# Optimization experiments

Hardware: AMD Instinct MI355X
Metric: run time of the kernel (lower is better)

Reference implementation:

```python
import jax, jax.numpy as jnp
import numpy as np

# --- fake-quant helpers (Brevitas INT quantization, straight-through in bwd) ---

def quant_weight_2bit(w):
    # symmetric signed 2-bit, narrow range: integer levels {-1, 0, 1}
    qmax = 1.0
    s = jnp.max(jnp.abs(jax.lax.stop_gradient(w))) / qmax
    r = jnp.clip(jnp.round(w / s), -qmax, qmax) * s
    return w + jax.lax.stop_gradient(r - w)  # STE


def quant_relu_2bit(x, max_val=6.0):
    # unsigned 2-bit activation quant: levels {0, 1, 2, 3} scaled to [0, max_val]
    n = 3.0  # 2**2 - 1
    s = max_val / n
    y = jnp.clip(x, 0.0, max_val)  # relu + clamp at max_val
    r = jnp.round(y / s) * s
    return y + jax.lax.stop_gradient(r - y)  # STE


def conv3x3_same(x, w):
    # NCHW input, OIHW weight, stride 1, padding 1
    return jax.lax.conv_general_dilated(
        x, w, window_strides=(1, 1), padding=((1, 1), (1, 1)),
        dimension_numbers=("NCHW", "OIHW", "NCHW"))


def maxpool2x2(x):
    return jax.lax.reduce_window(
        x, -jnp.inf, jax.lax.max,
        window_dimensions=(1, 1, 2, 2), window_strides=(1, 1, 2, 2),
        padding="VALID")


def setup_inputs() -> dict:
    key = jax.random.key(0)
    k0, k1, k2, k3 = jax.random.split(key, 4)
    B = 32768
    x = jax.random.normal(k0, (B, 1, 28, 28), dtype=jnp.float32)
    w1 = jax.random.normal(k1, (4, 1, 3, 3), dtype=jnp.float32) * 0.3
    w2 = jax.random.normal(k2, (4, 4, 3, 3), dtype=jnp.float32) * 0.2
    wf = jax.random.normal(k3, (10, 4 * 7 * 7), dtype=jnp.float32) * 0.1
    return {"x": x, "w1": w1, "w2": w2, "wf": wf}


def reference(x, w1, w2, wf):
    h = conv3x3_same(x, quant_weight_2bit(w1))        # [B,4,28,28]
    h = quant_relu_2bit(h)
    h = maxpool2x2(h)                                  # [B,4,14,14]
    h = conv3x3_same(h, quant_weight_2bit(w2))         # [B,4,14,14]
    h = quant_relu_2bit(h)
    h = maxpool2x2(h)                                  # [B,4,7,7]
    h = h.reshape(h.shape[0], -1)                      # [B,196]
    return h @ quant_weight_2bit(wf).T                 # [B,10]
```

## Files before the change

kernel.cpp:

```cpp
#include <hip/hip_runtime.h>

#define WSF_W1Q  0
#define WSF_SF2  36
#define WSI_W2P  0
#define WSI_L1   36
#define WSI_L3   37
#define WSI_L5   38
#define WSI_WFP  40

#define TOL2 4e-5f

__device__ __forceinline__ int dot4(int a, int b, int c) {
    return __builtin_amdgcn_sdot4(a, b, c, false);
}

__device__ __forceinline__ int pk_add16(int a, int b) {
    int r;
    asm("v_pk_add_i16 %0, %1, %2" : "=v"(r) : "v"(a), "v"(b));
    return r;
}

#define LDS_FENCE() asm volatile("s_waitcnt lgkmcnt(0)" ::: "memory")

__global__ void qweights_kernel(const float* __restrict__ w1,
                                const float* __restrict__ w2,
                                const float* __restrict__ wf,
                                float* __restrict__ wsf) {
    int* wsi = (int*)wsf + 64;
    const int lane = threadIdx.x;

    float m1 = 0.f, m2 = 0.f, mf = 0.f;
    if (lane < 36) m1 = fabsf(w1[lane]);
    for (int i = lane; i < 144; i += 64)  m2 = fmaxf(m2, fabsf(w2[i]));
    for (int i = lane; i < 1960; i += 64) mf = fmaxf(mf, fabsf(wf[i]));
    #pragma unroll
    for (int off = 32; off; off >>= 1) {
        m1 = fmaxf(m1, __shfl_xor(m1, off, 64));
        m2 = fmaxf(m2, __shfl_xor(m2, off, 64));
        mf = fmaxf(mf, __shfl_xor(mf, off, 64));
    }
    const float s1 = m1, s2 = m2, sf = mf;

    if (lane < 36) {
        double l = rint((double)w1[lane] / (double)s1);
        l = fmin(fmax(l, -1.0), 1.0);
        wsf[WSF_W1Q + lane] = (float)(l * (double)s1);
    }
    if (lane < 36) {
        int oc = lane / 9, tap = lane % 9;
        int dy = tap / 3, dx = tap % 3;
        int v = 0;
        for (int ic = 0; ic < 4; ++ic) {
            double l = rint((double)w2[((oc * 4 + ic) * 3 + dy) * 3 + dx] / (double)s2);
            l = fmin(fmax(l, -1.0), 1.0);
            v |= ((int)l & 0xFF) << (8 * ic);
        }
        wsi[WSI_W2P + lane] = v;
    }
    for (int u = lane; u < 49 * 12; u += 64) {
        int pix = u / 12, o = u - 12 * pix;
        int v = 0;
        if (o < 10) {
            for (int b = 0; b < 4; ++b) {
                double l = rint((double)wf[o * 196 + b * 49 + pix] / (double)sf);
                l = fmin(fmax(l, -1.0), 1.0);
                v |= ((int)l & 0xFF) << (8 * b);
            }
        }
        wsi[WSI_WFP + u] = v;
    }
    {
        double xa = 2.0 * (double)s2 * (double)lane;
        double xb = 2.0 * (double)s2 * (double)(lane + 64);
        double la = rint(fmin(fmax(xa, 0.0), 6.0) * 0.5);
        double lb = rint(fmin(fmax(xb, 0.0), 6.0) * 0.5);
        unsigned long long b1a = __ballot(la >= 1.0), b1b = __ballot(lb >= 1.0);
        unsigned long long b3a = __ballot(la >= 2.0), b3b = __ballot(lb >= 2.0);
        unsigned long long b5a = __ballot(la >= 3.0), b5b = __ballot(lb >= 3.0);
        if (lane == 0) {
            int L1 = b1a ? __ffsll(b1a) - 1 : (b1b ? 64 + __ffsll(b1b) - 1 : 4096);
            int L3 = b3a ? __ffsll(b3a) - 1 : (b3b ? 64 + __ffsll(b3b) - 1 : 4096);
            int L5 = b5a ? __ffsll(b5a) - 1 : (b5b ? 64 + __ffsll(b5b) - 1 : 4096);
            wsi[WSI_L1] = L1; wsi[WSI_L3] = L3; wsi[WSI_L5] = L5;
            wsf[WSF_SF2] = 2.0f * sf;
        }
    }
}

#define WAVES 4
#define P_IN 30
#define P_P1 18

__global__ __launch_bounds__(256, 8)
void fused_net_kernel(const float* __restrict__ x,
                      const float* __restrict__ wsf,
                      float* __restrict__ out, int B) {
    const int* wsi = (const int*)wsf + 64;

    __shared__ __align__(16) float s_in[WAVES][900];
    __shared__ __align__(16) int   s_p1[WAVES][16 * P_P1];
    __shared__ __align__(16) int   s_p2[WAVES][52];

    const int tid  = threadIdx.x;
    const int wave = tid >> 6;
    const int lane = tid & 63;
    const int img  = blockIdx.x * WAVES + wave;
    const bool act = (img < B);

    float* in_p = s_in[wave];
    int*   p1i  = s_p1[wave];
    int*   p2i  = s_p2[wave];
    const float* w1 = wsf + WSF_W1Q;

    {
        float4 zf = make_float4(0.f, 0.f, 0.f, 0.f);
        float4* z1 = (float4*)in_p;
        for (int t = lane; t < 225; t += 64) z1[t] = zf;
        int4 zi = make_int4(0, 0, 0, 0);
        int4* z2 = (int4*)p1i;
        for (int t = lane; t < 72; t += 64) z2[t] = zi;
    }
    LDS_FENCE();

    if (act) {
        const float4* xv = (const float4*)(x + (size_t)img * 784);
        for (int t = lane; t < 196; t += 64) {
            float4 v = xv[t];
            int row = t / 7;
            int c   = (t - row * 7) * 4;
            float* dst = in_p + (row + 1) * P_IN + c + 1;
            dst[0] = v.x; dst[1] = v.y; dst[2] = v.z; dst[3] = v.w;
        }
    }
    LDS_FENCE();

    if (act) {
        #pragma unroll 1
        for (int it = 0; it < 3; ++it) {
            const int t = lane + (it << 6);
            const int i = t / 14, j = t - i * 14;
            const float* base = in_p + (2 * i) * P_IN + 2 * j;
            float d[4][4];
            #pragma unroll
            for (int r = 0; r < 4; ++r) {
                float2 a = *(const float2*)(base + r * P_IN);
                float2 b = *(const float2*)(base + r * P_IN + 2);
                d[r][0] = a.x; d[r][1] = a.y; d[r][2] = b.x; d[r][3] = b.y;
            }
            float rr[4];
            float dmax = 0.f;
            #pragma unroll
            for (int oc = 0; oc < 4; ++oc) {
                float a00 = 0.f, a01 = 0.f, a10 = 0.f, a11 = 0.f;
                #pragma unroll
                for (int r = 0; r < 3; ++r)
                    #pragma unroll
                    for (int c = 0; c < 3; ++c) {
                        float wv = w1[oc * 9 + r * 3 + c];
                        a00 = fmaf(wv, d[r][c],         a00);
                        a01 = fmaf(wv, d[r][c + 1],     a01);
                        a10 = fmaf(wv, d[r + 1][c],     a10);
                        a11 = fmaf(wv, d[r + 1][c + 1], a11);
                    }
                float mx = fmaxf(fmaxf(a00, a01), fmaxf(a10, a11));
                float cc = fminf(fmaxf(0.5f * mx, 0.f), 3.f);
                float rv = rintf(cc);
                rr[oc] = rv;
                dmax = fmaxf(dmax, fabsf(cc - rv));
            }
            if (dmax > 0.5f - TOL2) {
                double dd[4][4];
                #pragma unroll
                for (int r = 0; r < 4; ++r)
                    #pragma unroll
                    for (int c = 0; c < 4; ++c) dd[r][c] = (double)d[r][c];
                #pragma unroll
                for (int oc = 0; oc < 4; ++oc) {
                    double a00 = 0, a01 = 0, a10 = 0, a11 = 0;
                    #pragma unroll
                    for (int r = 0; r < 3; ++r)
                        #pragma unroll
                        for (int c = 0; c < 3; ++c) {
                            double wv = (double)w1[oc * 9 + r * 3 + c];
                            a00 = fma(wv, dd[r][c],         a00);
                            a01 = fma(wv, dd[r][c + 1],     a01);
                            a10 = fma(wv, dd[r + 1][c],     a10);
                            a11 = fma(wv, dd[r + 1][c + 1], a11);
                        }
                    double mx = fmax(fmax(a00, a01), fmax(a10, a11));
                    rr[oc] = (float)rint(fmin(fmax(0.5 * mx, 0.0), 3.0));
                }
            }
            p1i[(i + 1) * P_P1 + (j + 1)] =
                (int)rr[0] | ((int)rr[1] << 8) | ((int)rr[2] << 16) | ((int)rr[3] << 24);
        }
        if (lane < 16) {
            const int px = 192 + (lane >> 2), oc = lane & 3;
            const int i = 13, j = px - 182;
            const float* base = in_p + (2 * i) * P_IN + 2 * j;
            float d[4][4];
            #pragma unroll
            for (int r = 0; r < 4; ++r) {
                float2 a = *(const float2*)(base + r * P_IN);
                float2 b = *(const float2*)(base + r * P_IN + 2);
                d[r][0] = a.x; d[r][1] = a.y; d[r][2] = b.x; d[r][3] = b.y;
            }
            const float* w9 = w1 + oc * 9;
            float a00 = 0.f, a01 = 0.f, a10 = 0.f, a11 = 0.f;
            #pragma unroll
            for (int r = 0; r < 3; ++r)
                #pragma unroll
                for (int c = 0; c < 3; ++c) {
                    float wv = w9[r * 3 + c];
                    a00 = fmaf(wv, d[r][c],         a00);
                    a01 = fmaf(wv, d[r][c + 1],     a01);
                    a10 = fmaf(wv, d[r + 1][c],     a10);
                    a11 = fmaf(wv, d[r + 1][c + 1], a11);
                }
            float mx = fmaxf(fmaxf(a00, a01), fmaxf(a10, a11));
            float cc = fminf(fmaxf(0.5f * mx, 0.f), 3.f);
            float rv = rintf(cc);
            if (fabsf(cc - rv) > 0.5f - TOL2) {
                double dd00 = 0, dd01 = 0, dd10 = 0, dd11 = 0;
                #pragma unroll
                for (int r = 0; r < 3; ++r)
                    #pragma unroll
                    for (int c = 0; c < 3; ++c) {
                        double wv = (double)w9[r * 3 + c];
                        dd00 = fma(wv, (double)d[r][c],         dd00);
                        dd01 = fma(wv, (double)d[r][c + 1],     dd01);
                        dd10 = fma(wv, (double)d[r + 1][c],     dd10);
                        dd11 = fma(wv, (double)d[r + 1][c + 1], dd11);
                    }
                double mxd = fmax(fmax(dd00, dd01), fmax(dd10, dd11));
                rv = (float)rint(fmin(fmax(0.5 * mxd, 0.0), 3.0));
            }
            int lv = (int)rv;
            int v = lv | (__shfl_xor(lv, 1, 64) << 8);
            v |= (__shfl_xor(v, 2, 64) << 16);
            if ((lane & 3) == 0)
                p1i[(i + 1) * P_P1 + (j + 1)] = v;
        }
    }
    LDS_FENCE();

    if (act && lane < 49) {
        const int i = lane / 7, j = lane - 7 * i;
        const int* bp = p1i + (2 * i) * P_P1 + 2 * j;
        int d[4][4];
        #pragma unroll
        for (int r = 0; r < 4; ++r) {
            int2 a = *(const int2*)(bp + r * P_P1);
            int2 b = *(const int2*)(bp + r * P_P1 + 2);
            d[r][0] = a.x; d[r][1] = a.y; d[r][2] = b.x; d[r][3] = b.y;
        }
        const int L1 = wsi[WSI_L1], L3 = wsi[WSI_L3], L5 = wsi[WSI_L5];
        int pk = 0;
        #pragma unroll
        for (int oc = 0; oc < 4; ++oc) {
            int a00 = 0, a01 = 0, a10 = 0, a11 = 0;
            #pragma unroll
            for (int r = 0; r < 3; ++r)
                #pragma unroll
                for (int c = 0; c < 3; ++c) {
                    int wv = wsi[WSI_W2P + oc * 9 + r * 3 + c];
                    a00 = dot4(d[r][c],         wv, a00);
                    a01 = dot4(d[r][c + 1],     wv, a01);
                    a10 = dot4(d[r + 1][c],     wv, a10);
                    a11 = dot4(d[r + 1][c + 1], wv, a11);
                }
            int mx = max(max(a00, a01), max(a10, a11));
            int lv = (mx >= L1) + (mx >= L3) + (mx >= L5);
            pk |= lv << (8 * oc);
        }
        p2i[lane] = pk;
    }
    LDS_FENCE();

    if (act) {
        int p[5] = {0, 0, 0, 0, 0};
        if (lane < 49) {
            int h4 = p2i[lane];
            const int* wr = wsi + WSI_WFP + lane * 12;
            int4 wa = *(const int4*)wr;
            int4 wb = *(const int4*)(wr + 4);
            int2 wc = *(const int2*)(wr + 8);
            int a0 = dot4(h4, wa.x, 0), a1 = dot4(h4, wa.y, 0);
            int a2 = dot4(h4, wa.z, 0), a3 = dot4(h4, wa.w, 0);
            int a4 = dot4(h4, wb.x, 0), a5 = dot4(h4, wb.y, 0);
            int a6 = dot4(h4, wb.z, 0), a7 = dot4(h4, wb.w, 0);
            int a8 = dot4(h4, wc.x, 0), a9 = dot4(h4, wc.y, 0);
            p[0] = (a0 << 16) | (a1 & 0xFFFF);
            p[1] = (a2 << 16) | (a3 & 0xFFFF);
            p[2] = (a4 << 16) | (a5 & 0xFFFF);
            p[3] = (a6 << 16) | (a7 & 0xFFFF);
            p[4] = (a8 << 16) | (a9 & 0xFFFF);
        }
        #pragma unroll
        for (int off = 32; off; off >>= 1) {
            #pragma unroll
            for (int k = 0; k < 5; ++k)
                p[k] = pk_add16(p[k], __shfl_xor(p[k], off, 64));
        }
        if (lane == 0) {
            const float sf2 = wsf[WSF_SF2];
            float2* op = (float2*)(out + (size_t)img * 10);
            #pragma unroll
            for (int k = 0; k < 5; ++k) {
                int hi = p[k] >> 16;
                int lo = (int)(short)(p[k] & 0xFFFF);
                op[k] = make_float2(sf2 * (float)hi, sf2 * (float)lo);
            }
        }
    }
}

extern "C" void kernel_launch(void* const* d_in, const int* in_sizes, int n_in,
                              void* d_out, int out_size, void* d_ws, size_t ws_size,
                              hipStream_t stream) {
    const float* x  = (const float*)d_in[0];
    const float* w1 = (const float*)d_in[1];
    const float* w2 = (const float*)d_in[2];
    const float* wf = (const float*)d_in[3];
    float* wsf = (float*)d_ws;
    float* out = (float*)d_out;

    const int B = in_sizes[0] / 784;

    qweights_kernel<<<1, 64, 0, stream>>>(w1, w2, wf, wsf);
    fused_net_kernel<<<(B + WAVES - 1) / WAVES, 256, 0, stream>>>(x, wsf, out, B);
}
```

Before: 197.8 us.

## Use packed FP32 FMA for conv1, zero only halos, widen weight-prep kernel

Conv1 is computed with v_pk_fma_f32 using a scalar-broadcast weight pair, so two output pixels are produced per instruction. Full zeroing of the padded LDS tiles is replaced by writing only the border cells, which also drops one LDS fence. The weight-quantization prep kernel moves from 64 to 256 threads with an LDS tree reduction. The inline-asm packed FMA requires the weight pair in SGPRs, which may force extra moves or fail if the weights are not uniform, and dropping the fence relies on later fences for ordering.

Measured after the change: 183.0 us. -7.5%, faster.

```diff
diff --git a/kernel.cpp b/kernel.cpp
--- a/kernel.cpp
+++ b/kernel.cpp
@@ -10,13 +10,19 @@
 
 #define TOL2 4e-5f
 
+typedef float v2f __attribute__((ext_vector_type(2)));
+
 __device__ __forceinline__ int dot4(int a, int b, int c) {
     return __builtin_amdgcn_sdot4(a, b, c, false);
 }
-
 __device__ __forceinline__ int pk_add16(int a, int b) {
     int r;
     asm("v_pk_add_i16 %0, %1, %2" : "=v"(r) : "v"(a), "v"(b));
+    return r;
+}
+__device__ __forceinline__ v2f pk_fma_sv(v2f ws, v2f d, v2f acc) {
+    v2f r;
+    asm("v_pk_fma_f32 %0, %1, %2, %3" : "=v"(r) : "s"(ws), "v"(d), "v"(acc));
     return r;
 }
 
@@ -27,27 +33,35 @@
                                 const float* __restrict__ wf,
                                 float* __restrict__ wsf) {
     int* wsi = (int*)wsf + 64;
-    const int lane = threadIdx.x;
-
-    float m1 = 0.f, m2 = 0.f, mf = 0.f;
-    if (lane < 36) m1 = fabsf(w1[lane]);
-    for (int i = lane; i < 144; i += 64)  m2 = fmaxf(m2, fabsf(w2[i]));
-    for (int i = lane; i < 1960; i += 64) mf = fmaxf(mf, fabsf(wf[i]));
-    #pragma unroll
-    for (int off = 32; off; off >>= 1) {
-        m1 = fmaxf(m1, __shfl_xor(m1, off, 64));
-        m2 = fmaxf(m2, __shfl_xor(m2, off, 64));
-        mf = fmaxf(mf, __shfl_xor(mf, off, 64));
-    }
-    const float s1 = m1, s2 = m2, sf = mf;
-
-    if (lane < 36) {
-        double l = rint((double)w1[lane] / (double)s1);
+    __shared__ float red[256];
+    const int tid = threadIdx.x;
+
+    float m = 0.f;
+    if (tid < 36) m = fabsf(w1[tid]);
+    red[tid] = m; __syncthreads();
+    for (int s = 128; s > 0; s >>= 1) { if (tid < s) red[tid] = fmaxf(red[tid], red[tid + s]); __syncthreads(); }
+    const float s1 = red[0]; __syncthreads();
+
+    m = 0.f;
+    if (tid < 144) m = fabsf(w2[tid]);
+    red[tid] = m; __syncthreads();
+    for (int s = 128; s > 0; s >>= 1) { if (tid < s) red[tid] = fmaxf(red[tid], red[tid + s]); __syncthreads(); }
+    const float s2 = red[0]; __syncthreads();
+
+    m = 0.f;
+    for (int i = tid; i < 1960; i += 256) m = fmaxf(m, fabsf(wf[i]));
+    red[tid] = m; __syncthreads();
+    for (int s = 128; s > 0; s >>= 1) { if (tid < s) red[tid] = fmaxf(red[tid], red[tid + s]); __syncthreads(); }
+    const float sf = red[0];
+
+    if (tid < 36) {
+        double l = rint((double)w1[tid] / (double)s1);
         l = fmin(fmax(l, -1.0), 1.0);
-        wsf[WSF_W1Q + lane] = (float)(l * (double)s1);
-    }
-    if (lane < 36) {
-        int oc = lane / 9, tap = lane % 9;
+        wsf[WSF_W1Q + tid] = (float)(l * (double)s1);
+    }
+    if (tid >= 64 && tid < 100) {
+        int u = tid - 64;
+        int oc = u / 9, tap = u % 9;
         int dy = tap / 3, dx = tap % 3;
         int v = 0;
         for (int ic = 0; ic < 4; ++ic) {
@@ -55,9 +69,9 @@
             l = fmin(fmax(l, -1.0), 1.0);
             v |= ((int)l & 0xFF) << (8 * ic);
         }
-        wsi[WSI_W2P + lane] = v;
-    }
-    for (int u = lane; u < 49 * 12; u += 64) {
+        wsi[WSI_W2P + u] = v;
+    }
+    for (int u = tid; u < 49 * 12; u += 256) {
         int pix = u / 12, o = u - 12 * pix;
         int v = 0;
         if (o < 10) {
@@ -69,7 +83,8 @@
         }
         wsi[WSI_WFP + u] = v;
     }
-    {
+    if (tid < 64) {
+        const int lane = tid;
         double xa = 2.0 * (double)s2 * (double)lane;
         double xb = 2.0 * (double)s2 * (double)(lane + 64);
         double la = rint(fmin(fmax(xa, 0.0), 6.0) * 0.5);
@@ -112,15 +127,16 @@
     int*   p2i  = s_p2[wave];
     const float* w1 = wsf + WSF_W1Q;
 
-    {
-        float4 zf = make_float4(0.f, 0.f, 0.f, 0.f);
-        float4* z1 = (float4*)in_p;
-        for (int t = lane; t < 225; t += 64) z1[t] = zf;
-        int4 zi = make_int4(0, 0, 0, 0);
-        int4* z2 = (int4*)p1i;
-        for (int t = lane; t < 72; t += 64) z2[t] = zi;
-    }
-    LDS_FENCE();
+    if (lane < 30) { in_p[lane] = 0.f; in_p[29 * 30 + lane] = 0.f; }
+    if (lane < 28) { in_p[(lane + 1) * 30] = 0.f; in_p[(lane + 1) * 30 + 29] = 0.f; }
+    if (lane < 60) {
+        int bi;
+        if (lane < 16)      bi = lane;
+        else if (lane < 32) bi = 15 * P_P1 + (lane - 16);
+        else if (lane < 46) bi = (lane - 31) * P_P1;
+        else                bi = (lane - 45) * P_P1 + 15;
+        p1i[bi] = 0;
+    }
 
     if (act) {
         const float4* xv = (const float4*)(x + (size_t)img * 784);
@@ -140,29 +156,33 @@
             const int t = lane + (it << 6);
             const int i = t / 14, j = t - i * 14;
             const float* base = in_p + (2 * i) * P_IN + 2 * j;
-            float d[4][4];
+            v2f A[4], S[4], Bp[4];
             #pragma unroll
             for (int r = 0; r < 4; ++r) {
-                float2 a = *(const float2*)(base + r * P_IN);
-                float2 b = *(const float2*)(base + r * P_IN + 2);
-                d[r][0] = a.x; d[r][1] = a.y; d[r][2] = b.x; d[r][3] = b.y;
+                const float* rp = base + r * P_IN;
+                A[r]  = *(const v2f*)rp;
+                Bp[r] = *(const v2f*)(rp + 2);
+                v2f s; s.x = rp[1]; s.y = rp[2];
+                S[r] = s;
             }
             float rr[4];
             float dmax = 0.f;
             #pragma unroll
             for (int oc = 0; oc < 4; ++oc) {
-                float a00 = 0.f, a01 = 0.f, a10 = 0.f, a11 = 0.f;
-                #pragma unroll
-                for (int r = 0; r < 3; ++r)
-                    #pragma unroll
-                    for (int c = 0; c < 3; ++c) {
-                        float wv = w1[oc * 9 + r * 3 + c];
-                        a00 = fmaf(wv, d[r][c],         a00);
-                        a01 = fmaf(wv, d[r][c + 1],     a01);
-                        a10 = fmaf(wv, d[r + 1][c],     a10);
-                        a11 = fmaf(wv, d[r + 1][c + 1], a11);
-                    }
-                float mx = fmaxf(fmaxf(a00, a01), fmaxf(a10, a11));
+                const float* w9 = w1 + oc * 9;
+                v2f acc01 = {0.f, 0.f}, acc23 = {0.f, 0.f};
+                #pragma unroll
+                for (int r = 0; r < 3; ++r) {
+                    float wa = w9[r * 3], wb = w9[r * 3 + 1], wc = w9[r * 3 + 2];
+                    v2f wav = {wa, wa}, wbv = {wb, wb}, wcv = {wc, wc};
+                    acc01 = pk_fma_sv(wav, A[r],      acc01);
+                    acc01 = pk_fma_sv(wbv, S[r],      acc01);
+                    acc01 = pk_fma_sv(wcv, Bp[r],     acc01);
+                    acc23 = pk_fma_sv(wav, A[r + 1],  acc23);
+                    acc23 = pk_fma_sv(wbv, S[r + 1],  acc23);
+                    acc23 = pk_fma_sv(wcv, Bp[r + 1], acc23);
+                }
+                float mx = fmaxf(fmaxf(acc01.x, acc01.y), fmaxf(acc23.x, acc23.y));
                 float cc = fminf(fmaxf(0.5f * mx, 0.f), 3.f);
                 float rv = rintf(cc);
                 rr[oc] = rv;
@@ -171,9 +191,10 @@
             if (dmax > 0.5f - TOL2) {
                 double dd[4][4];
                 #pragma unroll
-                for (int r = 0; r < 4; ++r)
-                    #pragma unroll
-                    for (int c = 0; c < 4; ++c) dd[r][c] = (double)d[r][c];
+                for (int r = 0; r < 4; ++r) {
+                    dd[r][0] = (double)A[r].x; dd[r][1] = (double)A[r].y;
+                    dd[r][2] = (double)Bp[r].x; dd[r][3] = (double)Bp[r].y;
+                }
                 #pragma unroll
                 for (int oc = 0; oc < 4; ++oc) {
                     double a00 = 0, a01 = 0, a10 = 0, a11 = 0;
@@ -327,6 +348,6 @@
 
     const int B = in_sizes[0] / 784;
 
-    qweights_kernel<<<1, 64, 0, stream>>>(w1, w2, wf, wsf);
+    qweights_kernel<<<1, 256, 0, stream>>>(w1, w2, wf, wsf);
     fused_net_kernel<<<(B + WAVES - 1) / WAVES, 256, 0, stream>>>(x, wsf, out, B);
 }
```
